# Kernel optimization log

Hardware: AMD Instinct MI355X
Metric: run time of the kernel (lower is better)

## Reference

```python
import jax, jax.numpy as jnp
import numpy as np
from jax import lax

T, B = 32, 32
GRID = (16, 16)
N_ACT = 5
CNN_DIM = 512
MAP_DIM = CNN_DIM + N_ACT  # 517
FLAT = MAP_DIM * GRID[0] * GRID[1]  # 132352


def _conv(x, w, b, stride):
    y = lax.conv_general_dilated(x, w, (stride, stride), 'VALID',
                                 dimension_numbers=('NCHW', 'OIHW', 'NCHW'))
    return jax.nn.relu(y + b[None, :, None, None])


def setup_inputs() -> dict:
    key = jax.random.key(0)
    ks = jax.random.split(key, 16)
    inp = {
        'image': jax.random.uniform(ks[0], (T * B, 3, 64, 64), jnp.float32),
        'last_action': jax.random.randint(ks[1], (T * B,), 0, N_ACT),
        'position': jax.random.randint(ks[2], (T * B, 2), 0, GRID[0]),
        'done': jnp.zeros((T, B), jnp.float32),
        'state0': jnp.zeros((B, MAP_DIM, GRID[0], GRID[1]), jnp.float32),
        'c1_w': jax.random.normal(ks[3], (32, 3, 8, 8), jnp.float32) * 0.05,
        'c1_b': jnp.zeros((32,), jnp.float32),
        'c2_w': jax.random.normal(ks[4], (64, 32, 4, 4), jnp.float32) * 0.05,
        'c2_b': jnp.zeros((64,), jnp.float32),
        'c3_w': jax.random.normal(ks[5], (64, 64, 3, 3), jnp.float32) * 0.05,
        'c3_b': jnp.zeros((64,), jnp.float32),
        'fc_w': jax.random.normal(ks[6], (CNN_DIM, 1024), jnp.float32) * 0.03,
        'fc_b': jnp.zeros((CNN_DIM,), jnp.float32),
        'pol_w1': jax.random.normal(ks[7], (64, FLAT), jnp.float32) * 0.005,
        'pol_b1': jnp.zeros((64,), jnp.float32),
        'pol_w2': jax.random.normal(ks[8], (N_ACT, 64), jnp.float32) * 0.01,
        'pol_b2': jnp.zeros((N_ACT,), jnp.float32),
        'val_w1': jax.random.normal(ks[9], (64, FLAT), jnp.float32) * 0.005,
        'val_b1': jnp.zeros((64,), jnp.float32),
        'val_w2': jax.random.normal(ks[10], (1, 64), jnp.float32) * 0.01,
        'val_b2': jnp.zeros((1,), jnp.float32),
    }
    return inp


def reference(image, last_action, position, done, state0,
              c1_w, c1_b, c2_w, c2_b, c3_w, c3_b, fc_w, fc_b,
              pol_w1, pol_b1, pol_w2, pol_b2, val_w1, val_b1, val_w2, val_b2):
    # NatureCNN feature extractor (image already normalized to [0,1])
    x = _conv(image, c1_w, c1_b, 4)   # (TB,32,15,15)
    x = _conv(x, c2_w, c2_b, 2)       # (TB,64,6,6)
    x = _conv(x, c3_w, c3_b, 1)       # (TB,64,4,4)
    feat = jax.nn.relu(x.reshape(x.shape[0], -1) @ fc_w.T + fc_b)  # (TB,512)
    onehot = jax.nn.one_hot(last_action, N_ACT, dtype=feat.dtype)
    h = jnp.concatenate([feat, onehot], axis=1)       # (TB,517)

    h_seq = h.reshape(T, B, MAP_DIM)
    idx_seq = position.reshape(T, B, 2)
    benv = jnp.arange(B)

    def step(state, inp):
        ht, dt, it = inp
        masked = (1.0 - dt)[:, None, None, None] * state      # reset done envs
        new_state = masked.at[benv, :, it[:, 0], it[:, 1]].set(ht)  # scatter write
        return new_state, new_state.reshape(B, -1)

    final_state, outs = lax.scan(step, state0, (h_seq, done, idx_seq))
    hidden = outs.reshape(T * B, FLAT)

    logits = jnp.tanh(hidden @ pol_w1.T + pol_b1) @ pol_w2.T + pol_b2  # (TB,5)
    v = jnp.tanh(hidden @ val_w1.T + val_b1) @ val_w2.T + val_b2       # (TB,1)
    return logits, v, final_state
```

## Files before the change

kernel.cpp:

```cpp
#include <hip/hip_runtime.h>

#define T_ 32
#define B_ 32
#define MAPD 517
#define P_ 256
#define FLATD (MAPD*P_)
#define TBN (T_*B_)

typedef unsigned short u16;
typedef unsigned int u32;
typedef __attribute__((ext_vector_type(4))) short short4v;
typedef __attribute__((ext_vector_type(8))) short short8v;
typedef __attribute__((ext_vector_type(4))) float f32x4;
typedef __attribute__((ext_vector_type(4))) u32 u32x4;

__device__ __forceinline__ float bfv(u16 u){ u32 x = ((u32)u)<<16; return __uint_as_float(x); }
__device__ __forceinline__ u16 fbf(float f){
  u32 x = __float_as_uint(f);
  return (u16)((x + 0x7fffu + ((x>>16)&1u))>>16);
}
template<bool F32> __device__ __forceinline__ float ld(const void* p, size_t i){
  if constexpr (F32) return ((const float*)p)[i];
  else               return bfv(((const u16*)p)[i]);
}

__global__ void k_probe(const void* img, int* flag){
  if (threadIdx.x == 0 && blockIdx.x == 0){
    const u16* u = (const u16*)img;
    int cnt = 0;
    for (int i = 0; i < 256; ++i) if (u[i] <= 0x4380u) ++cnt;
    *flag = (cnt < 240) ? 1 : 0;
  }
}

__global__ __launch_bounds__(256) void k_prep(const void* c1w, const void* c2w, const void* c3w,
                                              const void* fcw, const void* st0,
                                              u16* W1F, u16* W2F, u16* W3F, u16* FWF, u16* ST0T,
                                              const int* flag){
  __shared__ __align__(16) char smem_[32768];
  bool f32 = (*flag != 0);
  int bid = blockIdx.x, tid = threadIdx.x;
  if (bid < 24){
    int idx = bid*256 + tid;
    int j = idx & 7, l = (idx>>3) & 63, t = idx>>9;
    int nt = t/6, s = t - nt*6;
    int oc = nt*16 + (l&15);
    int kk = 8*(4*s + (l>>4)) + j;
    float v = f32 ? ((const float*)c1w)[oc*192+kk] : bfv(((const u16*)c1w)[oc*192+kk]);
    W1F[idx] = fbf(v);
  } else if (bid < 152){
    int idx = (bid-24)*256 + tid;
    int j = idx & 7, l = (idx>>3) & 63, s = (idx>>9) & 15, nt = idx>>13;
    int oc = nt*16 + (l&15);
    int cin = (l>>4)*8 + j;
    int src = oc*512 + cin*16 + (s>>2)*4 + (s&3);
    float v = f32 ? ((const float*)c2w)[src] : bfv(((const u16*)c2w)[src]);
    W2F[idx] = fbf(v);
  } else if (bid < 296){
    int idx = (bid-152)*256 + tid;
    int j = idx & 7, l = (idx>>3) & 63, t = idx>>9;
    int nt = t/18, s = t - nt*18;
    int oc = nt*16 + (l&15);
    int c = (s&1)*32 + (l>>4)*8 + j;
    int src = oc*576 + c*9 + (s>>1);
    float v = f32 ? ((const float*)c3w)[src] : bfv(((const u16*)c3w)[src]);
    W3F[idx] = fbf(v);
  } else if (bid < 424){
    int b = bid - 296;
    for (int it = 0; it < 16; ++it){
      int idx = (b*16 + it)*256 + tid;
      int j = idx & 7, l = (idx>>3) & 63, frag = idx >> 9;
      int nt = frag >> 5, kt = frag & 31;
      int kc = kt*32 + ((l>>4)<<3) + j;
      int kr = (kc & 63)*16 + (kc >> 6);
      int o  = nt*16 + (l & 15);
      float v = f32 ? ((const float*)fcw)[(size_t)o*1024 + kr]
                    : bfv(((const u16*)fcw)[(size_t)o*1024 + kr]);
      FWF[idx] = fbf(v);
    }
  } else {
    u16* tile = (u16*)smem_;
    int b0 = bid - 424;
    int c0 = (b0 >> 2)*8, p0 = (b0 & 3)*64;
    for (int it = 0; it < 64; ++it){
      int idx = it*256 + tid;
      int pl = idx & 63, b = (idx>>6)&31, ci = idx>>11;
      int c = c0 + ci;
      float v = 0.f;
      if (c < MAPD)
        v = f32 ? ((const float*)st0)[((size_t)b*MAPD+c)*256 + p0+pl]
                : bfv(((const u16*)st0)[((size_t)b*MAPD+c)*256 + p0+pl]);
      tile[ci*2048 + pl*32 + b] = fbf(v);
    }
    __syncthreads();
    for (int it = 0; it < 64; ++it){
      int idx = it*256 + tid;
      int b = idx & 31, ci = (idx>>5)&7, pl = idx>>8;
      int c = c0 + ci;
      if (c < MAPD)
        ST0T[((size_t)(p0+pl)*MAPD + c)*32 + b] = tile[ci*2048 + pl*32 + b];
    }
  }
}

__global__ void k_meta(const int* pos, const void* done, const int* lact,
                       int* prev, float* coef, float* H, int* lastw, float* lastc, const int* flag){
  bool f32 = (*flag != 0);
  int bid = blockIdx.x;
  if (bid < 4){
    int i = bid*256 + threadIdx.x;
    int t = i >> 5, b = i & 31;
    int p = pos[i*2]*16 + pos[i*2+1];
    int pv = -1;
    for (int s = t-1; s >= 0; --s){
      int n = s*32 + b;
      if (pos[n*2]*16 + pos[n*2+1] == p){ pv = s; break; }
    }
    float cf = 1.f;
    for (int s = (pv<0?0:pv+1); s <= t-1; ++s)
      cf *= (1.f - (f32 ? ((const float*)done)[s*32+b] : bfv(((const u16*)done)[s*32+b])));
    prev[i] = pv; coef[i] = cf;
    int la = lact[i];
    #pragma unroll
    for (int a = 0; a < 5; ++a) H[(size_t)i*MAPD + 512 + a] = (la == a) ? 1.f : 0.f;
  } else {
    int i = (bid-4)*256 + threadIdx.x;
    int b = i >> 8, p = i & 255;
    int lw = -1;
    for (int s = T_-1; s >= 0; --s){
      int n = s*32 + b;
      if (pos[n*2]*16 + pos[n*2+1] == p){ lw = s; break; }
    }
    float cf = 1.f;
    for (int s = (lw<0?0:lw+1); s < T_; ++s)
      cf *= (1.f - (f32 ? ((const float*)done)[s*32+b] : bfv(((const u16*)done)[s*32+b])));
    lastw[i] = lw; lastc[i] = cf;
  }
}

__global__ __launch_bounds__(256) void k_conv1(const void* img, const u16* W1F, const void* bias,
                                               u16* out, const int* flag){
  __shared__ u16 sImg[12288];
  __shared__ u16 sWF[6144];
  __shared__ float sB[32];
  bool f32 = (*flag != 0);
  int n = blockIdx.x, tid = threadIdx.x;
  if (f32){
    const float4* ip = (const float4*)((const float*)img + (size_t)n*12288);
    for (int i = tid; i < 3072; i += 256){
      float4 v = ip[i];
      ushort4 u; u.x = fbf(v.x); u.y = fbf(v.y); u.z = fbf(v.z); u.w = fbf(v.w);
      *(ushort4*)(sImg + i*4) = u;
    }
  } else {
    const ushort4* ip = (const ushort4*)((const u16*)img + (size_t)n*12288);
    for (int i = tid; i < 3072; i += 256) *(ushort4*)(sImg + i*4) = ip[i];
  }
  { const ushort4* wf = (const ushort4*)W1F;
    for (int i = tid; i < 1536; i += 256) *(ushort4*)(sWF + i*4) = wf[i]; }
  if (tid < 32) sB[tid] = f32 ? ((const float*)bias)[tid] : bfv(((const u16*)bias)[tid]);
  __syncthreads();

  int wv = tid >> 6, lane = tid & 63;
  int mi = lane & 15, q = lane >> 4;

  short8v bfr[2][6];
  #pragma unroll
  for (int nt = 0; nt < 2; ++nt)
    #pragma unroll
    for (int s = 0; s < 6; ++s)
      bfr[nt][s] = *(const short8v*)(sWF + ((nt*6+s)*64 + lane)*8);

  f32x4 acc[4][2];
  #pragma unroll
  for (int mt = 0; mt < 4; ++mt)
    #pragma unroll
    for (int nt = 0; nt < 2; ++nt)
      acc[mt][nt] = (f32x4){0.f,0.f,0.f,0.f};

  int base[4];
  #pragma unroll
  for (int mt = 0; mt < 4; ++mt){
    int m = (wv*4+mt)*16 + mi;
    int mc = m < 225 ? m : 224;
    int oy = mc/15, ox = mc - oy*15;
    base[mt] = oy*256 + ox*4;
  }

  for (int s = 0; s < 6; ++s){
    int cky = 4*s + q;
    int off = (cky >> 3)*4096 + (cky & 7)*64;
    #pragma unroll
    for (int mt = 0; mt < 4; ++mt){
      const u16* ap = sImg + base[mt] + off;
      short4v lo = *(const short4v*)ap;
      short4v hi = *(const short4v*)(ap + 4);
      short8v a = __builtin_shufflevector(lo, hi, 0,1,2,3,4,5,6,7);
      acc[mt][0] = __builtin_amdgcn_mfma_f32_16x16x32_bf16(a, bfr[0][s], acc[mt][0], 0,0,0);
      acc[mt][1] = __builtin_amdgcn_mfma_f32_16x16x32_bf16(a, bfr[1][s], acc[mt][1], 0,0,0);
    }
  }

  u16* ob = out + (size_t)n*7200;
  #pragma unroll
  for (int mt = 0; mt < 4; ++mt){
    int mrow0 = (wv*4+mt)*16 + q*4;
    #pragma unroll
    for (int nt = 0; nt < 2; ++nt){
      int oc = nt*16 + mi;
      float bv = sB[oc];
      #pragma unroll
      for (int r = 0; r < 4; ++r){
        int m = mrow0 + r;
        if (m < 225) ob[m*32 + oc] = fbf(fmaxf(acc[mt][nt][r] + bv, 0.f));
      }
    }
  }
}

__global__ __launch_bounds__(256) void k_conv2(const u16* __restrict__ A, const u16* __restrict__ W2F,
                                               const void* bias, u16* __restrict__ out, const int* flag){
  __shared__ u16 sIn[7200];
  bool f32 = (*flag != 0);
  int n = blockIdx.x, tid = threadIdx.x;
  const ushort4* ip = (const ushort4*)(A + (size_t)n*7200);
  for (int i = tid; i < 1800; i += 256) *(ushort4*)(sIn + i*4) = ip[i];
  int wv = tid >> 6, lane = tid & 63, mi = lane & 15, q = lane >> 4;

  short8v bfr[16];
  #pragma unroll
  for (int s = 0; s < 16; ++s)
    bfr[s] = ((const short8v*)W2F)[(wv*16+s)*64 + lane];

  int oc = wv*16 + mi;
  float bv = f32 ? ((const float*)bias)[oc] : bfv(((const u16*)bias)[oc]);
  f32x4 acc[3];
  #pragma unroll
  for (int mt = 0; mt < 3; ++mt) acc[mt] = (f32x4){0.f,0.f,0.f,0.f};
  int base[3];
  #pragma unroll
  for (int mt = 0; mt < 3; ++mt){
    int m = mt*16 + mi; if (m > 35) m = 35;
    int oy = m/6, ox = m - oy*6;
    base[mt] = (oy*30 + ox*2)*32;
  }
  __syncthreads();
  #pragma unroll
  for (int s = 0; s < 16; ++s){
    int off = ((s>>2)*15 + (s&3))*32 + q*8;
    #pragma unroll
    for (int mt = 0; mt < 3; ++mt){
      short8v a = *(const short8v*)(sIn + base[mt] + off);
      acc[mt] = __builtin_amdgcn_mfma_f32_16x16x32_bf16(a, bfr[s], acc[mt], 0,0,0);
    }
  }
  u16* ob = out + (size_t)n*2304;
  #pragma unroll
  for (int mt = 0; mt < 3; ++mt)
    #pragma unroll
    for (int r = 0; r < 4; ++r){
      int m = mt*16 + q*4 + r;
      if (m < 36) ob[m*64 + oc] = fbf(fmaxf(acc[mt][r] + bv, 0.f));
    }
}

__global__ __launch_bounds__(256) void k_conv3(const u16* __restrict__ Bv, const u16* __restrict__ W3F,
                                               const void* bias, u16* __restrict__ out, const int* flag){
  __shared__ u16 sIn[2304];
  bool f32 = (*flag != 0);
  int n = blockIdx.x, tid = threadIdx.x;
  const ushort4* ip = (const ushort4*)(Bv + (size_t)n*2304);
  for (int i = tid; i < 576; i += 256) *(ushort4*)(sIn + i*4) = ip[i];
  int wv = tid >> 6, lane = tid & 63, mi = lane & 15, q = lane >> 4;
  int oy = mi >> 2, ox = mi & 3;
  int oc = wv*16 + mi;
  float bv = f32 ? ((const float*)bias)[oc] : bfv(((const u16*)bias)[oc]);

  short8v bfr[18];
  #pragma unroll
  for (int s = 0; s < 18; ++s)
    bfr[s] = ((const short8v*)W3F)[(wv*18+s)*64 + lane];

  f32x4 acc = (f32x4){0.f,0.f,0.f,0.f};
  __syncthreads();
  #pragma unroll
  for (int s = 0; s < 18; ++s){
    int pair = s >> 1, ky = pair/3, kx = pair - ky*3;
    int off = ((oy+ky)*6 + ox+kx)*64 + (s&1)*32 + q*8;
    short8v a = *(const short8v*)(sIn + off);
    acc = __builtin_amdgcn_mfma_f32_16x16x32_bf16(a, bfr[s], acc, 0,0,0);
  }
  u16* ob = out + (size_t)n*1024;
  #pragma unroll
  for (int r = 0; r < 4; ++r)
    ob[(q*4+r)*64 + oc] = fbf(fmaxf(acc[r] + bv, 0.f));
}

__global__ __launch_bounds__(256) void k_fc(const u16* __restrict__ C, const u16* __restrict__ FWF,
                                            const void* fb, float* __restrict__ H, const int* flag){
  bool f32 = (*flag != 0);
  int wv = threadIdx.x >> 6, lane = threadIdx.x & 63;
  int mi = lane & 15, q = lane >> 4;
  int mt = blockIdx.x >> 3;
  int nt = (blockIdx.x & 7)*4 + wv;
  const u16* ap = C + (size_t)(mt*16 + mi)*1024 + q*8;
  const short8v* bp = (const short8v*)FWF + (size_t)nt*32*64 + lane;
  f32x4 acc0 = (f32x4){0.f,0.f,0.f,0.f};
  f32x4 acc1 = (f32x4){0.f,0.f,0.f,0.f};
  #pragma unroll
  for (int kt = 0; kt < 32; kt += 2){
    short8v a0 = *(const short8v*)(ap + kt*32);
    short8v b0 = bp[kt*64];
    short8v a1 = *(const short8v*)(ap + (kt+1)*32);
    short8v b1 = bp[(kt+1)*64];
    acc0 = __builtin_amdgcn_mfma_f32_16x16x32_bf16(a0, b0, acc0, 0,0,0);
    acc1 = __builtin_amdgcn_mfma_f32_16x16x32_bf16(a1, b1, acc1, 0,0,0);
  }
  int o = nt*16 + mi;
  float bv = f32 ? ((const float*)fb)[o] : bfv(((const u16*)fb)[o]);
  #pragma unroll
  for (int r = 0; r < 4; ++r){
    int m = mt*16 + q*4 + r;
    H[(size_t)m*MAPD + o] = fmaxf(acc0[r] + acc1[r] + bv, 0.f);
  }
}

template<bool F32> __device__ void wt_body(const void* pw1, const void* vw1, u16* wt, u32* tile){
  int c  = blockIdx.x >> 1;
  int ph = blockIdx.x & 1;
  for (int it = 0; it < 4; ++it){
    int idx = it*256 + threadIdx.x;
    int jp = idx >> 4, pg = idx & 15;
    int j0 = jp*2;
    const void* w = (j0 < 64) ? pw1 : vw1;
    int jj0 = (j0 < 64) ? j0 : j0-64;
    size_t base0 = (size_t)jj0*FLATD + c*P_ + ph*128 + pg*8;
    size_t base1 = base0 + FLATD;
    u16 a[8], b[8];
    if constexpr (F32){
      const float* f = (const float*)w;
      float4 a0 = *(const float4*)(f + base0), a1 = *(const float4*)(f + base0 + 4);
      float4 b0 = *(const float4*)(f + base1), b1 = *(const float4*)(f + base1 + 4);
      a[0]=fbf(a0.x); a[1]=fbf(a0.y); a[2]=fbf(a0.z); a[3]=fbf(a0.w);
      a[4]=fbf(a1.x); a[5]=fbf(a1.y); a[6]=fbf(a1.z); a[7]=fbf(a1.w);
      b[0]=fbf(b0.x); b[1]=fbf(b0.y); b[2]=fbf(b0.z); b[3]=fbf(b0.w);
      b[4]=fbf(b1.x); b[5]=fbf(b1.y); b[6]=fbf(b1.z); b[7]=fbf(b1.w);
    } else {
      short8v va = *(const short8v*)((const u16*)w + base0);
      short8v vb = *(const short8v*)((const u16*)w + base1);
      #pragma unroll
      for (int k = 0; k < 8; ++k){ a[k] = (u16)va[k]; b[k] = (u16)vb[k]; }
    }
    int slot = (jp >> 2) ^ pg;
    int sub  = jp & 3;
    #pragma unroll
    for (int k = 0; k < 8; ++k){
      int pp = pg*8 + k;
      tile[pp*64 + slot*4 + sub] = (u32)a[k] | ((u32)b[k] << 16);
    }
  }
  __syncthreads();
  for (int it = 0; it < 8; ++it){
    int idx = it*256 + threadIdx.x;
    int pp = idx >> 4, jb = idx & 15;
    int slot = jb ^ ((pp >> 3) & 15);
    u32x4 v = *(const u32x4*)(tile + pp*64 + slot*4);
    int p = ph*128 + pp;
    *(u32x4*)(wt + ((size_t)p*MAPD + c)*128 + jb*8) = v;
  }
}
__global__ __launch_bounds__(256) void k_wt(const void* pw1, const void* vw1, u16* wt, const int* flag){
  __shared__ u32 tile[128*64];
  if (*flag) wt_body<true>(pw1,vw1,wt,tile); else wt_body<false>(pw1,vw1,wt,tile);
}

template<int CLEN>
__device__ __forceinline__ void yloop(const u16* __restrict__ wp, const float* __restrict__ sSb,
                                      float (&acc)[8][2]){
  #pragma unroll 10
  for (int c = 0; c < CLEN; ++c){
    u32 w = *(const u32*)(wp + (size_t)c*128);
    float w0 = bfv((u16)(w & 0xffffu)), w1 = bfv((u16)(w >> 16));
    const float4* s4 = (const float4*)(sSb + c*32);
    float4 sa = s4[0], sb = s4[1];
    float sv[8] = {sa.x,sa.y,sa.z,sa.w,sb.x,sb.y,sb.z,sb.w};
    #pragma unroll
    for (int bb = 0; bb < 8; ++bb){
      acc[bb][0] += sv[bb]*w0;
      acc[bb][1] += sv[bb]*w1;
    }
  }
}
__global__ __launch_bounds__(256) void k_yinit(const u16* __restrict__ ST0T, const u16* __restrict__ wt,
                                               u16* __restrict__ PARTB){
  __shared__ float sS[130*32];
  int p = blockIdx.x >> 2, cq = blockIdx.x & 3;
  int c0 = cq*130;
  int clen = (cq == 3) ? 127 : 130;
  const ushort4* ssrc = (const ushort4*)(ST0T + ((size_t)p*MAPD + c0)*32);
  int n4 = clen*8;
  for (int i = threadIdx.x; i < n4; i += 256){
    ushort4 u = ssrc[i];
    float4 f; f.x = bfv(u.x); f.y = bfv(u.y); f.z = bfv(u.z); f.w = bfv(u.w);
    *(float4*)(sS + i*4) = f;
  }
  __syncthreads();
  int jg = threadIdx.x & 63, bg = threadIdx.x >> 6;
  int j0 = jg*2, b0 = bg*8;
  const u16* wp = wt + ((size_t)p*MAPD + c0)*128 + j0;
  float acc[8][2] = {};
  if (cq < 3) yloop<130>(wp, sS + b0, acc);
  else        yloop<127>(wp, sS + b0, acc);
  u32* op = (u32*)(PARTB + (size_t)blockIdx.x*4096);
  #pragma unroll
  for (int bb = 0; bb < 8; ++bb){
    u32 pk = (u32)fbf(acc[bb][0]) | ((u32)fbf(acc[bb][1]) << 16);
    op[((b0+bb)*128 + j0) >> 1] = pk;
  }
}

__global__ __launch_bounds__(256) void k_yred(const u16* __restrict__ PARTB, float* __restrict__ YI){
  int o = blockIdx.x*64 + (threadIdx.x & 63);
  int kq = threadIdx.x >> 6;
  float s = 0.f;
  const u16* pp = PARTB + (size_t)kq*256*4096 + o;
  #pragma unroll 8
  for (int k = 0; k < 256; ++k) s += bfv(pp[(size_t)k*4096]);
  __shared__ float red[256];
  red[threadIdx.x] = s;
  __syncthreads();
  if (threadIdx.x < 64)
    YI[o] = red[threadIdx.x] + red[threadIdx.x+64] + red[threadIdx.x+128] + red[threadIdx.x+192];
}

__global__ __launch_bounds__(128) void k_delta(const float* __restrict__ H, const u16* __restrict__ wt,
                                               const u16* __restrict__ st0t,
                                               const int* __restrict__ pos, const void* done,
                                               const int* __restrict__ prev, const float* __restrict__ coef,
                                               float* __restrict__ dlt4, const int* flag){
  __shared__ float diff[132];
  bool f32 = (*flag != 0);
  int n = blockIdx.x >> 2, cq = blockIdx.x & 3;
  int c0 = cq*130, clen = (cq == 3) ? 127 : 130;
  int b = n & 31;
  int p = pos[n*2]*16 + pos[n*2+1];
  float dn = f32 ? ((const float*)done)[n] : bfv(((const u16*)done)[n]);
  float m = 1.f - dn;
  int pv = prev[n];
  float cf = coef[n]*m;
  const float* hc = H + (size_t)n*MAPD + c0;
  for (int c = threadIdx.x; c < clen; c += 128){
    float old;
    if (pv >= 0) old = H[(size_t)(pv*32 + b)*MAPD + c0 + c];
    else         old = bfv(st0t[((size_t)p*MAPD + c0 + c)*32 + b]);
    diff[c] = hc[c] - cf*old;
  }
  __syncthreads();
  int j = threadIdx.x;
  const u16* wp = wt + ((size_t)p*MAPD + c0)*128 + j;
  float acc = 0.f;
  int c = 0;
  for (; c + 4 <= clen; c += 4){
    u16 w0 = wp[(size_t)c*128], w1 = wp[(size_t)(c+1)*128];
    u16 w2 = wp[(size_t)(c+2)*128], w3 = wp[(size_t)(c+3)*128];
    acc += diff[c]*bfv(w0) + diff[c+1]*bfv(w1) + diff[c+2]*bfv(w2) + diff[c+3]*bfv(w3);
  }
  for (; c < clen; ++c) acc += diff[c]*bfv(wp[(size_t)c*128]);
  dlt4[(size_t)blockIdx.x*128 + j] = acc;
}

template<bool F32> __device__ void scan_body(const float* yi, const float* dlt4, const void* done,
                                             const void* pb1, const void* vb1,
                                             const void* pw2, const void* pb2,
                                             const void* vw2, const void* vb2, void* out,
                                             float* th){
  int b = blockIdx.x, j = threadIdx.x;
  float y = yi[b*128 + j];
  float bias = (j < 64) ? ld<F32>(pb1, j) : ld<F32>(vb1, j-64);
  for (int t = 0; t < T_; ++t){
    int n = t*32 + b;
    float m = 1.f - ld<F32>(done, n);
    const float* dp = dlt4 + (size_t)n*4*128 + j;
    float d = dp[0] + dp[128] + dp[256] + dp[384];
    y = m*y + d;
    th[j] = tanhf(y + bias);
    __syncthreads();
    if (j < 5){
      float s = ld<F32>(pb2, j);
      for (int q = 0; q < 64; ++q) s += th[q]*ld<F32>(pw2, j*64 + q);
      if constexpr (F32) ((float*)out)[n*5 + j] = s; else ((u16*)out)[n*5 + j] = fbf(s);
    } else if (j == 5){
      float s = ld<F32>(vb2, 0);
      for (int q = 0; q < 64; ++q) s += th[64 + q]*ld<F32>(vw2, q);
      if constexpr (F32) ((float*)out)[5120 + n] = s; else ((u16*)out)[5120 + n] = fbf(s);
    }
    __syncthreads();
  }
}
__global__ __launch_bounds__(128) void k_scan(const float* yi, const float* dlt4, const void* done,
                                              const void* pb1, const void* vb1,
                                              const void* pw2, const void* pb2,
                                              const void* vw2, const void* vb2, void* out,
                                              const int* flag){
  __shared__ float th[128];
  if (*flag) scan_body<true>(yi,dlt4,done,pb1,vb1,pw2,pb2,vw2,vb2,out,th);
  else       scan_body<false>(yi,dlt4,done,pb1,vb1,pw2,pb2,vw2,vb2,out,th);
}

template<bool F32> __device__ void final_body(const float* H, const void* st0,
                                              const int* lastw, const float* lastc, void* out){
  size_t i = (size_t)blockIdx.x*256 + threadIdx.x;
  if (i >= (size_t)B_*FLATD) return;
  int b = (int)(i / FLATD);
  int r = (int)(i - (size_t)b*FLATD);
  int c = r >> 8, p = r & 255;
  int lw = lastw[b*256 + p];
  float lc = lastc[b*256 + p];
  float v;
  if (lw >= 0) v = H[(size_t)(lw*32 + b)*MAPD + c]*lc;
  else         v = ld<F32>(st0, i)*lc;
  if constexpr (F32) ((float*)out)[6144 + i] = v; else ((u16*)out)[6144 + i] = fbf(v);
}
__global__ __launch_bounds__(256) void k_final(const float* H, const void* st0,
                                               const int* lastw, const float* lastc, void* out,
                                               const int* flag){
  if (*flag) final_body<true>(H,st0,lastw,lastc,out); else final_body<false>(H,st0,lastw,lastc,out);
}

extern "C" void kernel_launch(void* const* d_in, const int* in_sizes, int n_in,
                              void* d_out, int out_size, void* d_ws, size_t ws_size,
                              hipStream_t stream) {
  (void)in_sizes; (void)n_in; (void)out_size; (void)ws_size;
  const void* image = d_in[0];
  const int*  lact  = (const int*)d_in[1];
  const int*  pos   = (const int*)d_in[2];
  const void* done  = d_in[3];
  const void* st0   = d_in[4];
  const void* c1w = d_in[5];  const void* c1b = d_in[6];
  const void* c2w = d_in[7];  const void* c2b = d_in[8];
  const void* c3w = d_in[9];  const void* c3b = d_in[10];
  const void* fcw = d_in[11]; const void* fcb = d_in[12];
  const void* pw1 = d_in[13]; const void* pb1 = d_in[14];
  const void* pw2 = d_in[15]; const void* pb2 = d_in[16];
  const void* vw1 = d_in[17]; const void* vb1 = d_in[18];
  const void* vw2 = d_in[19]; const void* vb2 = d_in[20];
  char* ws = (char*)d_ws;

  u16*   WT    = (u16*)  (ws + 0);
  u16*   A     = (u16*)  (ws + 0);
  u16*   Bv    = (u16*)  (ws + 14745600);
  u16*   C     = (u16*)  (ws + 19464192);
  float* H     = (float*)(ws + 33882368);
  float* YI    = (float*)(ws + 36000256);
  u16*   PARTB = (u16*)  (ws + 36016640);
  float* DLT4  = (float*)(ws + 36016640);
  int*   PREV  = (int*)  (ws + 44405248);
  float* COEF  = (float*)(ws + 44409344);
  int*   LASTW = (int*)  (ws + 44413440);
  float* LASTC = (float*)(ws + 44446208);
  int*   FLAG  = (int*)  (ws + 44478976);
  u16*   W1F   = (u16*)  (ws + 44479232);
  u16*   W2F   = (u16*)  (ws + 44491520);
  u16*   W3F   = (u16*)  (ws + 44557056);
  u16*   FWF   = (u16*)  (ws + 44630784);
  u16*   ST0T  = (u16*)  (ws + 45679360);

  k_probe<<<1, 64, 0, stream>>>(image, FLAG);
  k_prep <<<684, 256, 0, stream>>>(c1w, c2w, c3w, fcw, st0, W1F, W2F, W3F, FWF, ST0T, FLAG);
  k_meta <<<36, 256, 0, stream>>>(pos, done, lact, PREV, COEF, H, LASTW, LASTC, FLAG);
  k_conv1<<<1024, 256, 0, stream>>>(image, W1F, c1b, A, FLAG);
  k_conv2<<<1024, 256, 0, stream>>>(A, W2F, c2b, Bv, FLAG);
  k_conv3<<<1024, 256, 0, stream>>>(Bv, W3F, c3b, C, FLAG);
  k_fc   <<<512, 256, 0, stream>>>(C, FWF, fcb, H, FLAG);
  k_wt   <<<1034, 256, 0, stream>>>(pw1, vw1, WT, FLAG);
  k_yinit<<<1024, 256, 0, stream>>>(ST0T, WT, PARTB);
  k_yred <<<64, 256, 0, stream>>>(PARTB, YI);
  k_delta<<<4096, 128, 0, stream>>>(H, WT, ST0T, pos, done, PREV, COEF, DLT4, FLAG);
  k_scan <<<32, 128, 0, stream>>>(YI, DLT4, done, pb1, vb1, pw2, pb2, vw2, vb2, d_out, FLAG);
  k_final<<<16544, 256, 0, stream>>>(H, st0, LASTW, LASTC, d_out, FLAG);
}
```

Baseline: 387.9 us.

## Fuse conv layers into one kernel, split delta columns, move heads out of scan

Merges the three conv kernels into one kernel per image that keeps the conv1 and conv2 activations in shared memory, so those intermediates no longer make a round trip through global memory. The delta kernel now gives each thread two output columns loaded as packed 32-bit words and splits channels between two halves, giving eight partial sums instead of four. The serial scan now only writes the tanh activations, and the small policy and value head dot products move to a separate parallel kernel that reduces with wave shuffles. This removes per-step block barriers from the scan. In exchange it adds one more launch and an extra global buffer.

Result: faster. 363.8 us (-6.2%).

```diff
diff --git a/kernel.cpp b/kernel.cpp
--- a/kernel.cpp
+++ b/kernel.cpp
@@ -12,6 +12,7 @@
 typedef __attribute__((ext_vector_type(4))) short short4v;
 typedef __attribute__((ext_vector_type(8))) short short8v;
 typedef __attribute__((ext_vector_type(4))) float f32x4;
+typedef __attribute__((ext_vector_type(2))) float f32x2;
 typedef __attribute__((ext_vector_type(4))) u32 u32x4;
 
 __device__ __forceinline__ float bfv(u16 u){ u32 x = ((u32)u)<<16; return __uint_as_float(x); }
@@ -138,11 +139,14 @@
   }
 }
 
-__global__ __launch_bounds__(256) void k_conv1(const void* img, const u16* W1F, const void* bias,
-                                               u16* out, const int* flag){
+__global__ __launch_bounds__(256) void k_conv123(const void* img,
+                                                 const u16* __restrict__ W1F, const void* b1,
+                                                 const u16* __restrict__ W2F, const void* b2,
+                                                 const u16* __restrict__ W3F, const void* b3,
+                                                 u16* __restrict__ out, const int* flag){
   __shared__ u16 sImg[12288];
-  __shared__ u16 sWF[6144];
-  __shared__ float sB[32];
+  __shared__ u16 sA[7200];
+  __shared__ u16 sBv[2304];
   bool f32 = (*flag != 0);
   int n = blockIdx.x, tid = threadIdx.x;
   if (f32){
@@ -156,144 +160,122 @@
     const ushort4* ip = (const ushort4*)((const u16*)img + (size_t)n*12288);
     for (int i = tid; i < 3072; i += 256) *(ushort4*)(sImg + i*4) = ip[i];
   }
-  { const ushort4* wf = (const ushort4*)W1F;
-    for (int i = tid; i < 1536; i += 256) *(ushort4*)(sWF + i*4) = wf[i]; }
-  if (tid < 32) sB[tid] = f32 ? ((const float*)bias)[tid] : bfv(((const u16*)bias)[tid]);
-  __syncthreads();
-
   int wv = tid >> 6, lane = tid & 63;
   int mi = lane & 15, q = lane >> 4;
 
-  short8v bfr[2][6];
+  short8v bfr1[2][6];
   #pragma unroll
   for (int nt = 0; nt < 2; ++nt)
     #pragma unroll
     for (int s = 0; s < 6; ++s)
-      bfr[nt][s] = *(const short8v*)(sWF + ((nt*6+s)*64 + lane)*8);
-
-  f32x4 acc[4][2];
-  #pragma unroll
-  for (int mt = 0; mt < 4; ++mt)
-    #pragma unroll
-    for (int nt = 0; nt < 2; ++nt)
-      acc[mt][nt] = (f32x4){0.f,0.f,0.f,0.f};
-
-  int base[4];
-  #pragma unroll
-  for (int mt = 0; mt < 4; ++mt){
-    int m = (wv*4+mt)*16 + mi;
-    int mc = m < 225 ? m : 224;
-    int oy = mc/15, ox = mc - oy*15;
-    base[mt] = oy*256 + ox*4;
-  }
-
-  for (int s = 0; s < 6; ++s){
-    int cky = 4*s + q;
-    int off = (cky >> 3)*4096 + (cky & 7)*64;
+      bfr1[nt][s] = ((const short8v*)W1F)[(nt*6+s)*64 + lane];
+  float b1v[2];
+  #pragma unroll
+  for (int nt = 0; nt < 2; ++nt)
+    b1v[nt] = f32 ? ((const float*)b1)[nt*16+mi] : bfv(((const u16*)b1)[nt*16+mi]);
+  __syncthreads();
+
+  {
+    f32x4 acc[4][2];
+    #pragma unroll
+    for (int mt = 0; mt < 4; ++mt)
+      #pragma unroll
+      for (int nt = 0; nt < 2; ++nt)
+        acc[mt][nt] = (f32x4){0.f,0.f,0.f,0.f};
+    int base[4];
     #pragma unroll
     for (int mt = 0; mt < 4; ++mt){
-      const u16* ap = sImg + base[mt] + off;
-      short4v lo = *(const short4v*)ap;
-      short4v hi = *(const short4v*)(ap + 4);
-      short8v a = __builtin_shufflevector(lo, hi, 0,1,2,3,4,5,6,7);
-      acc[mt][0] = __builtin_amdgcn_mfma_f32_16x16x32_bf16(a, bfr[0][s], acc[mt][0], 0,0,0);
-      acc[mt][1] = __builtin_amdgcn_mfma_f32_16x16x32_bf16(a, bfr[1][s], acc[mt][1], 0,0,0);
-    }
-  }
-
-  u16* ob = out + (size_t)n*7200;
-  #pragma unroll
-  for (int mt = 0; mt < 4; ++mt){
-    int mrow0 = (wv*4+mt)*16 + q*4;
-    #pragma unroll
-    for (int nt = 0; nt < 2; ++nt){
-      int oc = nt*16 + mi;
-      float bv = sB[oc];
+      int m = (wv*4+mt)*16 + mi;
+      int mc = m < 225 ? m : 224;
+      int oy = mc/15, ox = mc - oy*15;
+      base[mt] = oy*256 + ox*4;
+    }
+    for (int s = 0; s < 6; ++s){
+      int cky = 4*s + q;
+      int off = (cky >> 3)*4096 + (cky & 7)*64;
+      #pragma unroll
+      for (int mt = 0; mt < 4; ++mt){
+        const u16* ap = sImg + base[mt] + off;
+        short4v lo = *(const short4v*)ap;
+        short4v hi = *(const short4v*)(ap + 4);
+        short8v a = __builtin_shufflevector(lo, hi, 0,1,2,3,4,5,6,7);
+        acc[mt][0] = __builtin_amdgcn_mfma_f32_16x16x32_bf16(a, bfr1[0][s], acc[mt][0], 0,0,0);
+        acc[mt][1] = __builtin_amdgcn_mfma_f32_16x16x32_bf16(a, bfr1[1][s], acc[mt][1], 0,0,0);
+      }
+    }
+    #pragma unroll
+    for (int mt = 0; mt < 4; ++mt){
+      int mrow0 = (wv*4+mt)*16 + q*4;
+      #pragma unroll
+      for (int nt = 0; nt < 2; ++nt){
+        int oc = nt*16 + mi;
+        #pragma unroll
+        for (int r = 0; r < 4; ++r){
+          int m = mrow0 + r;
+          if (m < 225) sA[m*32 + oc] = fbf(fmaxf(acc[mt][nt][r] + b1v[nt], 0.f));
+        }
+      }
+    }
+  }
+  __syncthreads();
+
+  {
+    short8v bfr2[16];
+    #pragma unroll
+    for (int s = 0; s < 16; ++s)
+      bfr2[s] = ((const short8v*)W2F)[(wv*16+s)*64 + lane];
+    int oc = wv*16 + mi;
+    float bv = f32 ? ((const float*)b2)[oc] : bfv(((const u16*)b2)[oc]);
+    f32x4 acc[3];
+    #pragma unroll
+    for (int mt = 0; mt < 3; ++mt) acc[mt] = (f32x4){0.f,0.f,0.f,0.f};
+    int base[3];
+    #pragma unroll
+    for (int mt = 0; mt < 3; ++mt){
+      int m = mt*16 + mi; if (m > 35) m = 35;
+      int oy = m/6, ox = m - oy*6;
+      base[mt] = (oy*30 + ox*2)*32;
+    }
+    #pragma unroll
+    for (int s = 0; s < 16; ++s){
+      int off = ((s>>2)*15 + (s&3))*32 + q*8;
+      #pragma unroll
+      for (int mt = 0; mt < 3; ++mt){
+        short8v a = *(const short8v*)(sA + base[mt] + off);
+        acc[mt] = __builtin_amdgcn_mfma_f32_16x16x32_bf16(a, bfr2[s], acc[mt], 0,0,0);
+      }
+    }
+    #pragma unroll
+    for (int mt = 0; mt < 3; ++mt)
       #pragma unroll
       for (int r = 0; r < 4; ++r){
-        int m = mrow0 + r;
-        if (m < 225) ob[m*32 + oc] = fbf(fmaxf(acc[mt][nt][r] + bv, 0.f));
+        int m = mt*16 + q*4 + r;
+        if (m < 36) sBv[m*64 + oc] = fbf(fmaxf(acc[mt][r] + bv, 0.f));
       }
-    }
-  }
-}
-
-__global__ __launch_bounds__(256) void k_conv2(const u16* __restrict__ A, const u16* __restrict__ W2F,
-                                               const void* bias, u16* __restrict__ out, const int* flag){
-  __shared__ u16 sIn[7200];
-  bool f32 = (*flag != 0);
-  int n = blockIdx.x, tid = threadIdx.x;
-  const ushort4* ip = (const ushort4*)(A + (size_t)n*7200);
-  for (int i = tid; i < 1800; i += 256) *(ushort4*)(sIn + i*4) = ip[i];
-  int wv = tid >> 6, lane = tid & 63, mi = lane & 15, q = lane >> 4;
-
-  short8v bfr[16];
-  #pragma unroll
-  for (int s = 0; s < 16; ++s)
-    bfr[s] = ((const short8v*)W2F)[(wv*16+s)*64 + lane];
-
-  int oc = wv*16 + mi;
-  float bv = f32 ? ((const float*)bias)[oc] : bfv(((const u16*)bias)[oc]);
-  f32x4 acc[3];
-  #pragma unroll
-  for (int mt = 0; mt < 3; ++mt) acc[mt] = (f32x4){0.f,0.f,0.f,0.f};
-  int base[3];
-  #pragma unroll
-  for (int mt = 0; mt < 3; ++mt){
-    int m = mt*16 + mi; if (m > 35) m = 35;
-    int oy = m/6, ox = m - oy*6;
-    base[mt] = (oy*30 + ox*2)*32;
-  }
-  __syncthreads();
-  #pragma unroll
-  for (int s = 0; s < 16; ++s){
-    int off = ((s>>2)*15 + (s&3))*32 + q*8;
-    #pragma unroll
-    for (int mt = 0; mt < 3; ++mt){
-      short8v a = *(const short8v*)(sIn + base[mt] + off);
-      acc[mt] = __builtin_amdgcn_mfma_f32_16x16x32_bf16(a, bfr[s], acc[mt], 0,0,0);
-    }
-  }
-  u16* ob = out + (size_t)n*2304;
-  #pragma unroll
-  for (int mt = 0; mt < 3; ++mt)
-    #pragma unroll
-    for (int r = 0; r < 4; ++r){
-      int m = mt*16 + q*4 + r;
-      if (m < 36) ob[m*64 + oc] = fbf(fmaxf(acc[mt][r] + bv, 0.f));
-    }
-}
-
-__global__ __launch_bounds__(256) void k_conv3(const u16* __restrict__ Bv, const u16* __restrict__ W3F,
-                                               const void* bias, u16* __restrict__ out, const int* flag){
-  __shared__ u16 sIn[2304];
-  bool f32 = (*flag != 0);
-  int n = blockIdx.x, tid = threadIdx.x;
-  const ushort4* ip = (const ushort4*)(Bv + (size_t)n*2304);
-  for (int i = tid; i < 576; i += 256) *(ushort4*)(sIn + i*4) = ip[i];
-  int wv = tid >> 6, lane = tid & 63, mi = lane & 15, q = lane >> 4;
-  int oy = mi >> 2, ox = mi & 3;
-  int oc = wv*16 + mi;
-  float bv = f32 ? ((const float*)bias)[oc] : bfv(((const u16*)bias)[oc]);
-
-  short8v bfr[18];
-  #pragma unroll
-  for (int s = 0; s < 18; ++s)
-    bfr[s] = ((const short8v*)W3F)[(wv*18+s)*64 + lane];
-
-  f32x4 acc = (f32x4){0.f,0.f,0.f,0.f};
-  __syncthreads();
-  #pragma unroll
-  for (int s = 0; s < 18; ++s){
-    int pair = s >> 1, ky = pair/3, kx = pair - ky*3;
-    int off = ((oy+ky)*6 + ox+kx)*64 + (s&1)*32 + q*8;
-    short8v a = *(const short8v*)(sIn + off);
-    acc = __builtin_amdgcn_mfma_f32_16x16x32_bf16(a, bfr[s], acc, 0,0,0);
-  }
-  u16* ob = out + (size_t)n*1024;
-  #pragma unroll
-  for (int r = 0; r < 4; ++r)
-    ob[(q*4+r)*64 + oc] = fbf(fmaxf(acc[r] + bv, 0.f));
+  }
+  __syncthreads();
+
+  {
+    int oy = mi >> 2, ox = mi & 3;
+    int oc = wv*16 + mi;
+    float bv = f32 ? ((const float*)b3)[oc] : bfv(((const u16*)b3)[oc]);
+    short8v bfr3[18];
+    #pragma unroll
+    for (int s = 0; s < 18; ++s)
+      bfr3[s] = ((const short8v*)W3F)[(wv*18+s)*64 + lane];
+    f32x4 acc = (f32x4){0.f,0.f,0.f,0.f};
+    #pragma unroll
+    for (int s = 0; s < 18; ++s){
+      int pair = s >> 1, ky = pair/3, kx = pair - ky*3;
+      int off = ((oy+ky)*6 + ox+kx)*64 + (s&1)*32 + q*8;
+      short8v a = *(const short8v*)(sBv + off);
+      acc = __builtin_amdgcn_mfma_f32_16x16x32_bf16(a, bfr3[s], acc, 0,0,0);
+    }
+    u16* ob = out + (size_t)n*1024;
+    #pragma unroll
+    for (int r = 0; r < 4; ++r)
+      ob[(q*4+r)*64 + oc] = fbf(fmaxf(acc[r] + bv, 0.f));
+  }
 }
 
 __global__ __launch_bounds__(256) void k_fc(const u16* __restrict__ C, const u16* __restrict__ FWF,
@@ -437,7 +419,7 @@
                                                const u16* __restrict__ st0t,
                                                const int* __restrict__ pos, const void* done,
                                                const int* __restrict__ prev, const float* __restrict__ coef,
-                                               float* __restrict__ dlt4, const int* flag){
+                                               float* __restrict__ dlt8, const int* flag){
   __shared__ float diff[132];
   bool f32 = (*flag != 0);
   int n = blockIdx.x >> 2, cq = blockIdx.x & 3;
@@ -456,55 +438,83 @@
     diff[c] = hc[c] - cf*old;
   }
   __syncthreads();
-  int j = threadIdx.x;
-  const u16* wp = wt + ((size_t)p*MAPD + c0)*128 + j;
-  float acc = 0.f;
+  int half = threadIdx.x >> 6, jp = threadIdx.x & 63, j0 = jp*2;
+  int hbase, hlen;
+  if (cq == 3){ hbase = half*64; hlen = half ? 63 : 64; }
+  else        { hbase = half*65; hlen = 65; }
+  const u16* wp = wt + ((size_t)p*MAPD + c0 + hbase)*128 + j0;
+  const float* dptr = diff + hbase;
+  float a0 = 0.f, a1 = 0.f;
   int c = 0;
-  for (; c + 4 <= clen; c += 4){
-    u16 w0 = wp[(size_t)c*128], w1 = wp[(size_t)(c+1)*128];
-    u16 w2 = wp[(size_t)(c+2)*128], w3 = wp[(size_t)(c+3)*128];
-    acc += diff[c]*bfv(w0) + diff[c+1]*bfv(w1) + diff[c+2]*bfv(w2) + diff[c+3]*bfv(w3);
-  }
-  for (; c < clen; ++c) acc += diff[c]*bfv(wp[(size_t)c*128]);
-  dlt4[(size_t)blockIdx.x*128 + j] = acc;
-}
-
-template<bool F32> __device__ void scan_body(const float* yi, const float* dlt4, const void* done,
-                                             const void* pb1, const void* vb1,
-                                             const void* pw2, const void* pb2,
-                                             const void* vw2, const void* vb2, void* out,
-                                             float* th){
+  for (; c + 4 <= hlen; c += 4){
+    u32 w0 = *(const u32*)(wp + (size_t)(c+0)*128);
+    u32 w1 = *(const u32*)(wp + (size_t)(c+1)*128);
+    u32 w2 = *(const u32*)(wp + (size_t)(c+2)*128);
+    u32 w3 = *(const u32*)(wp + (size_t)(c+3)*128);
+    float d0 = dptr[c], d1 = dptr[c+1], d2 = dptr[c+2], d3 = dptr[c+3];
+    a0 += d0*bfv((u16)(w0 & 0xffffu)) + d1*bfv((u16)(w1 & 0xffffu))
+        + d2*bfv((u16)(w2 & 0xffffu)) + d3*bfv((u16)(w3 & 0xffffu));
+    a1 += d0*bfv((u16)(w0 >> 16)) + d1*bfv((u16)(w1 >> 16))
+        + d2*bfv((u16)(w2 >> 16)) + d3*bfv((u16)(w3 >> 16));
+  }
+  for (; c < hlen; ++c){
+    u32 w = *(const u32*)(wp + (size_t)c*128);
+    a0 += dptr[c]*bfv((u16)(w & 0xffffu));
+    a1 += dptr[c]*bfv((u16)(w >> 16));
+  }
+  f32x2 st; st[0] = a0; st[1] = a1;
+  *(f32x2*)(dlt8 + ((size_t)blockIdx.x*2 + half)*128 + j0) = st;
+}
+
+__global__ __launch_bounds__(128) void k_scan(const float* __restrict__ yi,
+                                              const float* __restrict__ dlt8, const void* done,
+                                              const void* pb1, const void* vb1,
+                                              float* __restrict__ TH, const int* flag){
+  bool f32 = (*flag != 0);
   int b = blockIdx.x, j = threadIdx.x;
   float y = yi[b*128 + j];
-  float bias = (j < 64) ? ld<F32>(pb1, j) : ld<F32>(vb1, j-64);
+  float bias = (j < 64) ? (f32 ? ((const float*)pb1)[j]    : bfv(((const u16*)pb1)[j]))
+                        : (f32 ? ((const float*)vb1)[j-64] : bfv(((const u16*)vb1)[j-64]));
   for (int t = 0; t < T_; ++t){
     int n = t*32 + b;
-    float m = 1.f - ld<F32>(done, n);
-    const float* dp = dlt4 + (size_t)n*4*128 + j;
-    float d = dp[0] + dp[128] + dp[256] + dp[384];
+    float m = 1.f - (f32 ? ((const float*)done)[n] : bfv(((const u16*)done)[n]));
+    const float* dp = dlt8 + (size_t)n*1024 + j;
+    float d = dp[0] + dp[128] + dp[256] + dp[384]
+            + dp[512] + dp[640] + dp[768] + dp[896];
     y = m*y + d;
-    th[j] = tanhf(y + bias);
-    __syncthreads();
-    if (j < 5){
-      float s = ld<F32>(pb2, j);
-      for (int q = 0; q < 64; ++q) s += th[q]*ld<F32>(pw2, j*64 + q);
-      if constexpr (F32) ((float*)out)[n*5 + j] = s; else ((u16*)out)[n*5 + j] = fbf(s);
-    } else if (j == 5){
-      float s = ld<F32>(vb2, 0);
-      for (int q = 0; q < 64; ++q) s += th[64 + q]*ld<F32>(vw2, q);
-      if constexpr (F32) ((float*)out)[5120 + n] = s; else ((u16*)out)[5120 + n] = fbf(s);
-    }
-    __syncthreads();
-  }
-}
-__global__ __launch_bounds__(128) void k_scan(const float* yi, const float* dlt4, const void* done,
-                                              const void* pb1, const void* vb1,
-                                              const void* pw2, const void* pb2,
-                                              const void* vw2, const void* vb2, void* out,
-                                              const int* flag){
-  __shared__ float th[128];
-  if (*flag) scan_body<true>(yi,dlt4,done,pb1,vb1,pw2,pb2,vw2,vb2,out,th);
-  else       scan_body<false>(yi,dlt4,done,pb1,vb1,pw2,pb2,vw2,vb2,out,th);
+    TH[(size_t)n*128 + j] = tanhf(y + bias);
+  }
+}
+
+__global__ __launch_bounds__(256) void k_heads(const float* __restrict__ TH,
+                                               const void* pw2, const void* pb2,
+                                               const void* vw2, const void* vb2,
+                                               void* out, const int* flag){
+  bool f32 = (*flag != 0);
+  int wv = threadIdx.x >> 6, lane = threadIdx.x & 63;
+  int n = blockIdx.x*4 + wv;
+  const float* th = TH + (size_t)n*128;
+  float tq = th[lane];
+  float tv = th[64 + lane];
+  float acc[6];
+  #pragma unroll
+  for (int j = 0; j < 5; ++j)
+    acc[j] = tq * (f32 ? ((const float*)pw2)[j*64 + lane] : bfv(((const u16*)pw2)[j*64 + lane]));
+  acc[5] = tv * (f32 ? ((const float*)vw2)[lane] : bfv(((const u16*)vw2)[lane]));
+  #pragma unroll
+  for (int off = 32; off > 0; off >>= 1)
+    #pragma unroll
+    for (int j = 0; j < 6; ++j)
+      acc[j] += __shfl_down(acc[j], off, 64);
+  if (lane == 0){
+    #pragma unroll
+    for (int j = 0; j < 5; ++j){
+      float s = acc[j] + (f32 ? ((const float*)pb2)[j] : bfv(((const u16*)pb2)[j]));
+      if (f32) ((float*)out)[n*5 + j] = s; else ((u16*)out)[n*5 + j] = fbf(s);
+    }
+    float s = acc[5] + (f32 ? ((const float*)vb2)[0] : bfv(((const u16*)vb2)[0]));
+    if (f32) ((float*)out)[5120 + n] = s; else ((u16*)out)[5120 + n] = fbf(s);
+  }
 }
 
 template<bool F32> __device__ void final_body(const float* H, const void* st0,
@@ -547,13 +557,11 @@
   char* ws = (char*)d_ws;
 
   u16*   WT    = (u16*)  (ws + 0);
-  u16*   A     = (u16*)  (ws + 0);
-  u16*   Bv    = (u16*)  (ws + 14745600);
   u16*   C     = (u16*)  (ws + 19464192);
   float* H     = (float*)(ws + 33882368);
   float* YI    = (float*)(ws + 36000256);
   u16*   PARTB = (u16*)  (ws + 36016640);
-  float* DLT4  = (float*)(ws + 36016640);
+  float* DLT8  = (float*)(ws + 36016640);
   int*   PREV  = (int*)  (ws + 44405248);
   float* COEF  = (float*)(ws + 44409344);
   int*   LASTW = (int*)  (ws + 44413440);
@@ -564,18 +572,18 @@
   u16*   W3F   = (u16*)  (ws + 44557056);
   u16*   FWF   = (u16*)  (ws + 44630784);
   u16*   ST0T  = (u16*)  (ws + 45679360);
+  float* TH    = (float*)(ws + 54149888);
 
   k_probe<<<1, 64, 0, stream>>>(image, FLAG);
   k_prep <<<684, 256, 0, stream>>>(c1w, c2w, c3w, fcw, st0, W1F, W2F, W3F, FWF, ST0T, FLAG);
   k_meta <<<36, 256, 0, stream>>>(pos, done, lact, PREV, COEF, H, LASTW, LASTC, FLAG);
-  k_conv1<<<1024, 256, 0, stream>>>(image, W1F, c1b, A, FLAG);
-  k_conv2<<<1024, 256, 0, stream>>>(A, W2F, c2b, Bv, FLAG);
-  k_conv3<<<1024, 256, 0, stream>>>(Bv, W3F, c3b, C, FLAG);
+  k_conv123<<<1024, 256, 0, stream>>>(image, W1F, c1b, W2F, c2b, W3F, c3b, C, FLAG);
   k_fc   <<<512, 256, 0, stream>>>(C, FWF, fcb, H, FLAG);
   k_wt   <<<1034, 256, 0, stream>>>(pw1, vw1, WT, FLAG);
   k_yinit<<<1024, 256, 0, stream>>>(ST0T, WT, PARTB);
   k_yred <<<64, 256, 0, stream>>>(PARTB, YI);
-  k_delta<<<4096, 128, 0, stream>>>(H, WT, ST0T, pos, done, PREV, COEF, DLT4, FLAG);
-  k_scan <<<32, 128, 0, stream>>>(YI, DLT4, done, pb1, vb1, pw2, pb2, vw2, vb2, d_out, FLAG);
+  k_delta<<<4096, 128, 0, stream>>>(H, WT, ST0T, pos, done, PREV, COEF, DLT8, FLAG);
+  k_scan <<<32, 128, 0, stream>>>(YI, DLT8, done, pb1, vb1, TH, FLAG);
+  k_heads<<<256, 256, 0, stream>>>(TH, pw2, pb2, vw2, vb2, d_out, FLAG);
   k_final<<<16544, 256, 0, stream>>>(H, st0, LASTW, LASTC, d_out, FLAG);
 }
```
